# Optimization experiments

Hardware: AMD Instinct MI355X
Metric: run time of the kernel (lower is better)

## Reference

```python
import jax, jax.numpy as jnp
import numpy as np

B, S, D = 4, 2048, 1024
H = 16
DH = D // H  # 64


def setup_inputs() -> dict:
    key = jax.random.key(0)
    ks = jax.random.split(key, 9)
    s = 0.02
    return {
        "x": jax.random.normal(ks[0], (B, S, D), dtype=jnp.float32),
        "Wq": jax.random.normal(ks[1], (D, D), dtype=jnp.float32) * s,
        "bq": jnp.zeros((D,), dtype=jnp.float32),
        "Wk": jax.random.normal(ks[2], (D, D), dtype=jnp.float32) * s,
        "bk": jnp.zeros((D,), dtype=jnp.float32),
        "Wv": jax.random.normal(ks[3], (D, D), dtype=jnp.float32) * s,
        "bv": jnp.zeros((D,), dtype=jnp.float32),
        "Wp": jax.random.normal(ks[4], (D, D), dtype=jnp.float32) * s,
        "bp": jnp.zeros((D,), dtype=jnp.float32),
    }


def reference(x, Wq, bq, Wk, bk, Wv, bv, Wp, bp):
    b, s, d = x.shape
    # projections (torch Linear: x @ W.T + b)
    q = (x @ Wq.T + bq).reshape(b, s, H, DH).transpose(0, 2, 1, 3)   # [B,H,S,DH]
    # quirk faithful to source: key viewed as (B,S,DH,H) then transpose(1,3) -> [B,H,DH,S]
    k = (x @ Wk.T + bk).reshape(b, s, DH, H).transpose(0, 3, 2, 1)   # [B,H,DH,S]
    v = (x @ Wv.T + bv).reshape(b, s, H, DH).transpose(0, 2, 1, 3)   # [B,H,S,DH]

    scale = 1.0 / np.sqrt(DH).astype(np.float32)
    scores = jnp.einsum('bhqd,bhds->bhqs', q, k) * scale             # [B,H,S,S]
    causal = jnp.tril(jnp.ones((s, s), dtype=bool))
    scores = jnp.where(causal, scores, -jnp.inf)
    attn = jax.nn.softmax(scores, axis=-1)
    out = jnp.einsum('bhqs,bhsd->bhqd', attn, v)                      # [B,H,S,DH]
    out = out.transpose(0, 2, 1, 3).reshape(b, s, d)                  # [B,S,D]
    return out @ Wp.T + bp
```

## Files before the change

kernel.cpp:

```cpp
#include <hip/hip_runtime.h>
#include <cstdint>

#define B_  4
#define S_  2048
#define D_  1024
#define H_  16
#define DH_ 64

typedef unsigned short u16;
typedef __attribute__((ext_vector_type(8))) __bf16 bf16x8;
typedef __attribute__((ext_vector_type(4))) float f32x4;
typedef __attribute__((ext_vector_type(2))) uint32_t u32x2;

__device__ __forceinline__ u16 f2bf(float f) {
    union { float f; uint32_t u; } v; v.f = f;
    uint32_t r = (v.u + 0x7FFFu + ((v.u >> 16) & 1u)) >> 16;
    return (u16)r;
}
__device__ __forceinline__ u16 f2bf_fast(float f) {
    union { float f; uint32_t u; } v; v.f = f;
    return (u16)((v.u + 0x8000u) >> 16);
}
__device__ __forceinline__ uint32_t cvtpk(float lo, float hi) {
    uint32_t r;
    asm("v_cvt_pk_bf16_f32 %0, %1, %2" : "=v"(r) : "v"(lo), "v"(hi));
    return r;
}
__device__ __forceinline__ void gl2lds16(const void* g, void* l) {
    __builtin_amdgcn_global_load_lds(
        (const __attribute__((address_space(1))) void*)g,
        (__attribute__((address_space(3))) void*)l,
        16, 0, 0);
}

__global__ __launch_bounds__(256) void cvt_kernel(
    const float* __restrict__ x,  const float* __restrict__ wq,
    const float* __restrict__ wk, const float* __restrict__ wv,
    const float* __restrict__ wp,
    u16* __restrict__ xb, u16* __restrict__ wqb, u16* __restrict__ wkb,
    u16* __restrict__ wvb, u16* __restrict__ wpb)
{
    int bid = blockIdx.x;
    const float* src; u16* dst; int base;
    if (bid < 8192) {
        src = x; dst = xb; base = bid;
    } else {
        int w = (bid - 8192) >> 10;
        base  = (bid - 8192) & 1023;
        switch (w) {
            case 0: src = wq; dst = wqb; break;
            case 1: src = wk; dst = wkb; break;
            case 2: src = wv; dst = wvb; break;
            default: src = wp; dst = wpb; break;
        }
    }
    size_t i4 = (size_t)base * 256 + threadIdx.x;
    float4 v = *(const float4*)(src + i4 * 4);
    ushort4 o;
    o.x = f2bf(v.x); o.y = f2bf(v.y); o.z = f2bf(v.z); o.w = f2bf(v.w);
    *(ushort4*)(dst + i4 * 4) = o;
}

__device__ __forceinline__ void stage_tiles(
    u16* dA, u16* dB,
    const u16* __restrict__ X, const u16* __restrict__ W,
    int m0, int n0, int k0, int kperm, int wave, int lane)
{
#pragma unroll
    for (int t = 0; t < 4; ++t) {
        int idx = wave * 256 + t * 64 + lane;
        int row = idx >> 3, scc = idx & 7;
        int cg  = scc ^ (row & 7);
        gl2lds16(X + (size_t)(m0 + row) * 1024 + k0 + cg * 8,
                 &dA[(wave * 256 + t * 64) * 8]);
    }
#pragma unroll
    for (int t = 0; t < 4; ++t) {
        int idx = wave * 256 + t * 64 + lane;
        int row = idx >> 3, scc = idx & 7;
        int cg  = scc ^ (row & 7);
        int n   = n0 + row;
        int wr  = kperm ? ((n & 63) * 16 + (n >> 6)) : n;
        gl2lds16(W + (size_t)wr * 1024 + k0 + cg * 8,
                 &dB[(wave * 256 + t * 64) * 8]);
    }
}

__device__ __forceinline__ void gemm_core(
    u16* sA, u16* sB,
    const u16* __restrict__ X, const u16* __restrict__ W,
    const float* __restrict__ bias,
    u16* __restrict__ out_bf, float* __restrict__ out_f,
    int m0, int n0, int kperm, int mode, float scale)
{
    const int tid  = threadIdx.x;
    const int lane = tid & 63;
    const int wave = tid >> 6;
    const int l16  = lane & 15, l4 = lane >> 4;

    f32x4 acc[4][4];
#pragma unroll
    for (int i = 0; i < 4; ++i)
#pragma unroll
        for (int j = 0; j < 4; ++j)
            acc[i][j] = (f32x4){0.f, 0.f, 0.f, 0.f};

    const int wm = (wave >> 1) * 64;
    const int wn = (wave & 1) * 64;

    stage_tiles(sA, sB, X, W, m0, n0, 0, kperm, wave, lane);
    __syncthreads();

    int cur = 0;
#pragma unroll 1
    for (int t = 0; t < 16; ++t) {
        if (t < 15)
            stage_tiles(sA + (cur ^ 1) * 8192, sB + (cur ^ 1) * 8192,
                        X, W, m0, n0, (t + 1) * 64, kperm, wave, lane);

        const u16* cA = sA + cur * 8192;
        const u16* cB = sB + cur * 8192;
#pragma unroll
        for (int kk = 0; kk < 2; ++kk) {
            bf16x8 a[4], b[4];
#pragma unroll
            for (int i = 0; i < 4; ++i) {
                int row = wm + i * 16 + l16;
                int ch  = (kk * 4 + l4) ^ (row & 7);
                a[i] = *(const bf16x8*)&cA[row * 64 + ch * 8];
            }
#pragma unroll
            for (int j = 0; j < 4; ++j) {
                int row = wn + j * 16 + l16;
                int ch  = (kk * 4 + l4) ^ (row & 7);
                b[j] = *(const bf16x8*)&cB[row * 64 + ch * 8];
            }
#pragma unroll
            for (int i = 0; i < 4; ++i)
#pragma unroll
                for (int j = 0; j < 4; ++j)
                    acc[i][j] = __builtin_amdgcn_mfma_f32_16x16x32_bf16(
                        a[i], b[j], acc[i][j], 0, 0, 0);
        }
        __syncthreads();
        cur ^= 1;
    }

    float bj[4];
#pragma unroll
    for (int j = 0; j < 4; ++j) {
        int n  = n0 + wn + j * 16 + l16;
        int wr = kperm ? ((n & 63) * 16 + (n >> 6)) : n;
        bj[j]  = bias[wr];
    }
#pragma unroll
    for (int i = 0; i < 4; ++i) {
#pragma unroll
        for (int j = 0; j < 4; ++j) {
#pragma unroll
            for (int r = 0; r < 4; ++r) {
                int m = m0 + wm + i * 16 + l4 * 4 + r;
                int n = n0 + wn + j * 16 + l16;
                float v = (acc[i][j][r] + bj[j]) * scale;
                int bb = m >> 11, s = m & 2047;
                int h = n >> 6, dh = n & 63;
                if (mode == 1) {
                    out_bf[(((size_t)bb * H_ + h) * S_ + s) * DH_ + dh] = f2bf(v);
                } else if (mode == 2) {
                    out_bf[(((size_t)bb * H_ + h) * DH_ + dh) * S_ + s] = f2bf(v);
                } else {
                    out_f[(size_t)m * 1024 + n] = v;
                }
            }
        }
    }
}

__global__ __launch_bounds__(256, 2) void qkv_kernel(
    const u16* __restrict__ xb,
    const u16* __restrict__ Wqb, const float* __restrict__ bq,
    const u16* __restrict__ Wkb, const float* __restrict__ bk,
    const u16* __restrict__ Wvb, const float* __restrict__ bv,
    u16* __restrict__ Q, u16* __restrict__ K, u16* __restrict__ V)
{
    __shared__ __align__(16) u16 sA[2 * 128 * 64];
    __shared__ __align__(16) u16 sB[2 * 128 * 64];
    int swz = (blockIdx.x & 7) * 192 + (blockIdx.x >> 3);
    int x = swz & 7, y = (swz >> 3) & 63, z = swz >> 9;
    int n0 = x * 128, m0 = y * 128;
    const u16* W = (z == 0) ? Wqb : (z == 1) ? Wkb : Wvb;
    const float* bi = (z == 0) ? bq : (z == 1) ? bk : bv;
    u16* out = (z == 0) ? Q : (z == 1) ? K : V;
    const float c = 0.18033688011112042f;
    gemm_core(sA, sB, xb, W, bi, out, nullptr, m0, n0,
              (z == 1) ? 1 : 0, (z == 2) ? 2 : 1, (z == 0) ? c : 1.0f);
}

__global__ __launch_bounds__(256, 2) void proj_kernel(
    const u16* __restrict__ Ob, const u16* __restrict__ Wpb,
    const float* __restrict__ bp, float* __restrict__ out)
{
    __shared__ __align__(16) u16 sA[2 * 128 * 64];
    __shared__ __align__(16) u16 sB[2 * 128 * 64];
    int swz = (blockIdx.x & 7) * 64 + (blockIdx.x >> 3);
    int x = swz & 7, y = swz >> 3;
    gemm_core(sA, sB, Ob, Wpb, bp, nullptr, out,
              y * 128, x * 128, 0, 0, 1.0f);
}

#define LDP 72
__global__ __launch_bounds__(256, 4) void attn_flash(
    const u16* __restrict__ Q, const u16* __restrict__ K,
    const u16* __restrict__ Vt, u16* __restrict__ O)
{
    const int tid  = threadIdx.x;
    const int lane = tid & 63;
    const int wave = tid >> 6;
    const int l16  = lane & 15, l4 = lane >> 4;
    int swz = (blockIdx.x & 7) * 128 + (blockIdx.x >> 3);
    const int qt   = swz & 15;
    const int bh   = swz >> 4;

    __shared__ __align__(16) u16 sK[64 * LDP];
    __shared__ __align__(16) u16 sVt[64 * LDP];
    __shared__ __align__(16) u16 sP[4][16 * LDP];

    const int b = bh >> 4, h = bh & 15;

    const int srow = tid >> 3, scc = tid & 7;
    const u16* Kbase = K  + (size_t)bh * S_ * DH_;
    const u16* Vbase = Vt + (size_t)bh * DH_ * S_;

#pragma unroll 1
    for (int half = 0; half < 2; ++half) {
        const int q0 = (half ? (31 - qt) : qt) * 64;

        bf16x8 aq[2];
        {
            const u16* qp = Q + ((size_t)bh * S_ + q0 + wave * 16 + l16) * DH_ + l4 * 8;
            aq[0] = *(const bf16x8*)qp;
            aq[1] = *(const bf16x8*)(qp + 32);
        }

        float lsum = 0.f;
        f32x4 o[4];
#pragma unroll
        for (int dt = 0; dt < 4; ++dt) o[dt] = (f32x4){0.f, 0.f, 0.f, 0.f};

        uint4 pk0, pk1, pv0, pv1;
        pk0 = *(const uint4*)(Kbase + (size_t)(srow)      * DH_ + scc * 8);
        pk1 = *(const uint4*)(Kbase + (size_t)(srow + 32) * DH_ + scc * 8);
        pv0 = *(const uint4*)(Vbase + (size_t)(srow)      * S_  + scc * 8);
        pv1 = *(const uint4*)(Vbase + (size_t)(srow + 32) * S_  + scc * 8);

        for (int k0 = 0; k0 <= q0; k0 += 64) {
            *(uint4*)&sK [(srow)      * LDP + scc * 8] = pk0;
            *(uint4*)&sK [(srow + 32) * LDP + scc * 8] = pk1;
            *(uint4*)&sVt[(srow)      * LDP + scc * 8] = pv0;
            *(uint4*)&sVt[(srow + 32) * LDP + scc * 8] = pv1;
            if (k0 + 64 <= q0) {
                int kn = k0 + 64;
                pk0 = *(const uint4*)(Kbase + (size_t)(kn + srow)      * DH_ + scc * 8);
                pk1 = *(const uint4*)(Kbase + (size_t)(kn + srow + 32) * DH_ + scc * 8);
                pv0 = *(const uint4*)(Vbase + (size_t)(srow)      * S_ + kn + scc * 8);
                pv1 = *(const uint4*)(Vbase + (size_t)(srow + 32) * S_ + kn + scc * 8);
            }
            __syncthreads();

            f32x4 ts[4];
#pragma unroll
            for (int ct = 0; ct < 4; ++ct) {
                f32x4 sacc = (f32x4){0.f, 0.f, 0.f, 0.f};
#pragma unroll
                for (int kk = 0; kk < 2; ++kk) {
                    bf16x8 ak = *(const bf16x8*)&sK[(ct * 16 + l16) * LDP + kk * 32 + l4 * 8];
                    sacc = __builtin_amdgcn_mfma_f32_16x16x32_bf16(ak, aq[kk], sacc, 0, 0, 0);
                }
                ts[ct] = sacc;
            }

            if (k0 == q0) {
#pragma unroll
                for (int ct = 0; ct < 4; ++ct)
#pragma unroll
                    for (int r = 0; r < 4; ++r) {
                        int key = ct * 16 + l4 * 4 + r;
                        int qr  = wave * 16 + l16;
                        if (key > qr) ts[ct][r] = -1e30f;
                    }
            }

            uint32_t pw[4][2];
#pragma unroll
            for (int ct = 0; ct < 4; ++ct) {
                float p0 = exp2f(ts[ct][0]);
                float p1 = exp2f(ts[ct][1]);
                float p2 = exp2f(ts[ct][2]);
                float p3 = exp2f(ts[ct][3]);
                lsum += (p0 + p1) + (p2 + p3);
                pw[ct][0] = cvtpk(p0, p1);
                pw[ct][1] = cvtpk(p2, p3);
            }
#pragma unroll
            for (int ct = 0; ct < 4; ++ct)
                *(u32x2*)&sP[wave][l16 * LDP + ct * 16 + l4 * 4] =
                    *(const u32x2*)pw[ct];
            asm volatile("s_waitcnt lgkmcnt(0)" ::: "memory");

#pragma unroll
            for (int kk = 0; kk < 2; ++kk) {
                bf16x8 ap = *(const bf16x8*)&sP[wave][l16 * LDP + kk * 32 + l4 * 8];
#pragma unroll
                for (int dt = 0; dt < 4; ++dt) {
                    bf16x8 bv = *(const bf16x8*)&sVt[(dt * 16 + l16) * LDP + kk * 32 + l4 * 8];
                    o[dt] = __builtin_amdgcn_mfma_f32_16x16x32_bf16(ap, bv, o[dt], 0, 0, 0);
                }
            }
            __syncthreads();
        }

        lsum += __shfl_xor(lsum, 16, 64);
        lsum += __shfl_xor(lsum, 32, 64);
        float linv = 1.0f / lsum;
        float inv[4];
#pragma unroll
        for (int r = 0; r < 4; ++r) inv[r] = __shfl(linv, (l4 << 2) + r, 16);

#pragma unroll
        for (int dt = 0; dt < 4; ++dt) {
#pragma unroll
            for (int r = 0; r < 4; ++r) {
                int s  = q0 + wave * 16 + l4 * 4 + r;
                int dh = dt * 16 + l16;
                O[((size_t)b * S_ + s) * D_ + h * 64 + dh] = f2bf_fast(o[dt][r] * inv[r]);
            }
        }
    }
}

extern "C" void kernel_launch(void* const* d_in, const int* in_sizes, int n_in,
                              void* d_out, int out_size, void* d_ws, size_t ws_size,
                              hipStream_t stream) {
    const float* x  = (const float*)d_in[0];
    const float* Wq = (const float*)d_in[1];
    const float* bq = (const float*)d_in[2];
    const float* Wk = (const float*)d_in[3];
    const float* bk = (const float*)d_in[4];
    const float* Wv = (const float*)d_in[5];
    const float* bv = (const float*)d_in[6];
    const float* Wp = (const float*)d_in[7];
    const float* bp = (const float*)d_in[8];

    u16* ws = (u16*)d_ws;
    const size_t xel = (size_t)B_ * S_ * D_;
    const size_t wel = (size_t)D_ * D_;
    u16* xb  = ws;
    u16* Wqb = xb + xel;
    u16* Wkb = Wqb + wel;
    u16* Wvb = Wkb + wel;
    u16* Wpb = Wvb + wel;
    u16* Q   = Wpb + wel;
    u16* Kb  = Q + xel;
    u16* Vtb = Kb + xel;
    u16* Ob  = Vtb + xel;

    cvt_kernel<<<dim3(12288), dim3(256), 0, stream>>>(
        x, Wq, Wk, Wv, Wp, xb, Wqb, Wkb, Wvb, Wpb);
    qkv_kernel<<<dim3(1536), dim3(256), 0, stream>>>(
        xb, Wqb, bq, Wkb, bk, Wvb, bv, Q, Kb, Vtb);
    attn_flash<<<dim3(1024), dim3(256), 0, stream>>>(Q, Kb, Vtb, Ob);
    proj_kernel<<<dim3(512), dim3(256), 0, stream>>>(Ob, Wpb, bp, (float*)d_out);
}
```

Before: 283.2 us.

## Triple-buffer GEMM loads with 256x128 tiles, 512 threads and one barrier per step

```diff
diff --git a/kernel.cpp b/kernel.cpp
--- a/kernel.cpp
+++ b/kernel.cpp
@@ -61,32 +61,36 @@
     *(ushort4*)(dst + i4 * 4) = o;
 }
 
-__device__ __forceinline__ void stage_tiles(
+
+#define A_SLOT (256 * 64)
+#define B_SLOT (128 * 64)
+
+__device__ __forceinline__ void stage_unit(
     u16* dA, u16* dB,
     const u16* __restrict__ X, const u16* __restrict__ W,
     int m0, int n0, int k0, int kperm, int wave, int lane)
 {
 #pragma unroll
-    for (int t = 0; t < 4; ++t) {
-        int idx = wave * 256 + t * 64 + lane;
+    for (int rnd = 0; rnd < 4; ++rnd) {
+        int idx = rnd * 512 + wave * 64 + lane;
         int row = idx >> 3, scc = idx & 7;
         int cg  = scc ^ (row & 7);
         gl2lds16(X + (size_t)(m0 + row) * 1024 + k0 + cg * 8,
-                 &dA[(wave * 256 + t * 64) * 8]);
-    }
-#pragma unroll
-    for (int t = 0; t < 4; ++t) {
-        int idx = wave * 256 + t * 64 + lane;
+                 &dA[(rnd * 512 + wave * 64) * 8]);
+    }
+#pragma unroll
+    for (int rnd = 0; rnd < 2; ++rnd) {
+        int idx = rnd * 512 + wave * 64 + lane;
         int row = idx >> 3, scc = idx & 7;
         int cg  = scc ^ (row & 7);
         int n   = n0 + row;
         int wr  = kperm ? ((n & 63) * 16 + (n >> 6)) : n;
         gl2lds16(W + (size_t)wr * 1024 + k0 + cg * 8,
-                 &dB[(wave * 256 + t * 64) * 8]);
-    }
-}
-
-__device__ __forceinline__ void gemm_core(
+                 &dB[(rnd * 512 + wave * 64) * 8]);
+    }
+}
+
+__device__ __forceinline__ void gemm_pipe(
     u16* sA, u16* sB,
     const u16* __restrict__ X, const u16* __restrict__ W,
     const float* __restrict__ bias,
@@ -97,6 +101,8 @@
     const int lane = tid & 63;
     const int wave = tid >> 6;
     const int l16  = lane & 15, l4 = lane >> 4;
+    const int wm = (wave >> 1) * 64;
+    const int wn = (wave & 1) * 64;
 
     f32x4 acc[4][4];
 #pragma unroll
@@ -105,21 +111,25 @@
         for (int j = 0; j < 4; ++j)
             acc[i][j] = (f32x4){0.f, 0.f, 0.f, 0.f};
 
-    const int wm = (wave >> 1) * 64;
-    const int wn = (wave & 1) * 64;
-
-    stage_tiles(sA, sB, X, W, m0, n0, 0, kperm, wave, lane);
-    __syncthreads();
+    stage_unit(sA,          sB,         X, W, m0, n0, 0,  kperm, wave, lane);
+    stage_unit(sA + A_SLOT, sB + B_SLOT, X, W, m0, n0, 64, kperm, wave, lane);
+    asm volatile("s_waitcnt vmcnt(6)" ::: "memory");
+    __builtin_amdgcn_sched_barrier(0);
+    __builtin_amdgcn_s_barrier();
+    __builtin_amdgcn_sched_barrier(0);
 
     int cur = 0;
 #pragma unroll 1
     for (int t = 0; t < 16; ++t) {
-        if (t < 15)
-            stage_tiles(sA + (cur ^ 1) * 8192, sB + (cur ^ 1) * 8192,
-                        X, W, m0, n0, (t + 1) * 64, kperm, wave, lane);
-
-        const u16* cA = sA + cur * 8192;
-        const u16* cB = sB + cur * 8192;
+        int wsl = cur + 2; if (wsl >= 3) wsl -= 3;
+        int k2 = (t + 2 < 16) ? (t + 2) * 64 : 960;
+        stage_unit(sA + wsl * A_SLOT, sB + wsl * B_SLOT,
+                   X, W, m0, n0, k2, kperm, wave, lane);
+        asm volatile("" ::: "memory");
+
+        const u16* cA = sA + cur * A_SLOT;
+        const u16* cB = sB + cur * B_SLOT;
+        __builtin_amdgcn_s_setprio(1);
 #pragma unroll
         for (int kk = 0; kk < 2; ++kk) {
             bf16x8 a[4], b[4];
@@ -142,8 +152,12 @@
                     acc[i][j] = __builtin_amdgcn_mfma_f32_16x16x32_bf16(
                         a[i], b[j], acc[i][j], 0, 0, 0);
         }
-        __syncthreads();
-        cur ^= 1;
+        __builtin_amdgcn_s_setprio(0);
+        asm volatile("s_waitcnt vmcnt(6)" ::: "memory");
+        __builtin_amdgcn_sched_barrier(0);
+        __builtin_amdgcn_s_barrier();
+        __builtin_amdgcn_sched_barrier(0);
+        cur += 1; if (cur >= 3) cur = 0;
     }
 
     float bj[4];
@@ -176,36 +190,38 @@
     }
 }
 
-__global__ __launch_bounds__(256, 2) void qkv_kernel(
+__global__ __launch_bounds__(512, 2) void qkv_kernel(
     const u16* __restrict__ xb,
     const u16* __restrict__ Wqb, const float* __restrict__ bq,
     const u16* __restrict__ Wkb, const float* __restrict__ bk,
     const u16* __restrict__ Wvb, const float* __restrict__ bv,
     u16* __restrict__ Q, u16* __restrict__ K, u16* __restrict__ V)
 {
-    __shared__ __align__(16) u16 sA[2 * 128 * 64];
-    __shared__ __align__(16) u16 sB[2 * 128 * 64];
-    int swz = (blockIdx.x & 7) * 192 + (blockIdx.x >> 3);
-    int x = swz & 7, y = (swz >> 3) & 63, z = swz >> 9;
-    int n0 = x * 128, m0 = y * 128;
+    __shared__ __align__(16) u16 sA[3 * A_SLOT];
+    __shared__ __align__(16) u16 sB[3 * B_SLOT];
+    int swz = (blockIdx.x & 7) * 96 + (blockIdx.x >> 3);
+    int z = swz >> 8;
+    int rem = swz & 255;
+    int y = rem >> 3, x = rem & 7;
+    int m0 = y * 256, n0 = x * 128;
     const u16* W = (z == 0) ? Wqb : (z == 1) ? Wkb : Wvb;
     const float* bi = (z == 0) ? bq : (z == 1) ? bk : bv;
     u16* out = (z == 0) ? Q : (z == 1) ? K : V;
     const float c = 0.18033688011112042f;
-    gemm_core(sA, sB, xb, W, bi, out, nullptr, m0, n0,
+    gemm_pipe(sA, sB, xb, W, bi, out, nullptr, m0, n0,
               (z == 1) ? 1 : 0, (z == 2) ? 2 : 1, (z == 0) ? c : 1.0f);
 }
 
-__global__ __launch_bounds__(256, 2) void proj_kernel(
+__global__ __launch_bounds__(512, 2) void proj_kernel(
     const u16* __restrict__ Ob, const u16* __restrict__ Wpb,
     const float* __restrict__ bp, float* __restrict__ out)
 {
-    __shared__ __align__(16) u16 sA[2 * 128 * 64];
-    __shared__ __align__(16) u16 sB[2 * 128 * 64];
-    int swz = (blockIdx.x & 7) * 64 + (blockIdx.x >> 3);
-    int x = swz & 7, y = swz >> 3;
-    gemm_core(sA, sB, Ob, Wpb, bp, nullptr, out,
-              y * 128, x * 128, 0, 0, 1.0f);
+    __shared__ __align__(16) u16 sA[3 * A_SLOT];
+    __shared__ __align__(16) u16 sB[3 * B_SLOT];
+    int swz = (blockIdx.x & 7) * 32 + (blockIdx.x >> 3);
+    int y = swz >> 3, x = swz & 7;
+    gemm_pipe(sA, sB, Ob, Wpb, bp, nullptr, out,
+              y * 256, x * 128, 0, 0, 1.0f);
 }
 
 #define LDP 72
@@ -366,8 +382,8 @@
 
     cvt_kernel<<<dim3(12288), dim3(256), 0, stream>>>(
         x, Wq, Wk, Wv, Wp, xb, Wqb, Wkb, Wvb, Wpb);
-    qkv_kernel<<<dim3(1536), dim3(256), 0, stream>>>(
+    qkv_kernel<<<dim3(768), dim3(512), 0, stream>>>(
         xb, Wqb, bq, Wkb, bk, Wvb, bv, Q, Kb, Vtb);
     attn_flash<<<dim3(1024), dim3(256), 0, stream>>>(Q, Kb, Vtb, Ob);
-    proj_kernel<<<dim3(512), dim3(256), 0, stream>>>(Ob, Wpb, bp, (float*)d_out);
-}
+    proj_kernel<<<dim3(256), dim3(512), 0, stream>>>(Ob, Wpb, bp, (float*)d_out);
+}
```

Result: slower. 304.3 us (+7.5%).
